# Kernel tuning notes

Measured on AMD Instinct MI355X. Metric: run time of the kernel, lower is better.

Reference implementation:

```python
import jax, jax.numpy as jnp
import numpy as np

DIM_HEAD = 128
HEADS = 16
SCALE = DIM_HEAD ** -0.5


def rotate_half(t):
    # '... (j d) -> ... j d' with j=2: split into first/second halves
    x1, x2 = jnp.split(t, 2, axis=-1)
    return jnp.concatenate((-x2, x1), axis=-1)


def apply_rope(pos, t):
    # pos: [n, d]; t: [..., n, d]
    return t * jnp.cos(pos) + rotate_half(t) * jnp.sin(pos)


def setup_inputs() -> dict:
    key = jax.random.key(0)
    k0, k1, k2, k3 = jax.random.split(key, 4)
    b, n, dim = 2, 2048, 2048
    inner = HEADS * DIM_HEAD
    return {
        "x": jax.random.normal(k0, (b, n, dim), jnp.float32),
        "Wq": jax.random.normal(k1, (dim, inner), jnp.float32) * 0.02,
        "Wkv": jax.random.normal(k2, (dim, 2 * DIM_HEAD), jnp.float32) * 0.02,
        "Wout": jax.random.normal(k3, (inner, dim), jnp.float32) * 0.02,
    }


def reference(x, Wq, Wkv, Wout):
    b, n, dim = x.shape
    # projections from the UN-normalized x (norm in original is dead code)
    q = x @ Wq                               # [b, n, h*d]
    kv = x @ Wkv                             # [b, n, 2d]
    k, v = jnp.split(kv, 2, axis=-1)         # each [b, n, d] (multi-query)
    q = q.reshape(b, n, HEADS, DIM_HEAD).transpose(0, 2, 1, 3)  # [b,h,n,d]

    # rotary positions
    inv_freq = 1.0 / (10000.0 ** (jnp.arange(0, DIM_HEAD, 2, dtype=jnp.float32) / DIM_HEAD))
    freqs = jnp.arange(n, dtype=jnp.float32)[:, None] * inv_freq[None, :]
    pos = jnp.concatenate((freqs, freqs), axis=-1)  # [n, d]

    q = apply_rope(pos, q) * SCALE
    k = apply_rope(pos, k)

    sim = jnp.einsum('bhid,bjd->bhij', q, k)  # [b,h,n,n]
    causal_mask = jnp.triu(jnp.ones((n, n), dtype=bool), 1)
    neg = -jnp.finfo(sim.dtype).max
    sim = jnp.where(causal_mask, neg, sim)
    sim = sim - jax.lax.stop_gradient(jnp.max(sim, axis=-1, keepdims=True))
    attn = jax.nn.softmax(sim, axis=-1)

    out = jnp.einsum('bhij,bjd->bhid', attn, v)          # [b,h,n,d]
    out = out.transpose(0, 2, 1, 3).reshape(b, n, HEADS * DIM_HEAD)
    return out @ Wout
```

## Files before the change

kernel.cpp:

```cpp
#include <hip/hip_runtime.h>
#include <hip/hip_bf16.h>
#include <cstddef>
#include <cstdint>

#define BATCH 2
#define SEQ   2048
#define DIM   2048
#define HEADS 16
#define DHEAD 128
#define INNER (HEADS * DHEAD)
#define MROWS (BATCH * SEQ)
#define ATT_SCALE 0.08838834764831845f
#define QK_SCALE (0.08838834764831845f * 1.4426950408889634f)
#define NEG_LOG2_10000_DIV64 (-13.287712379549449f / 64.0f)
#define M_HAT 12.0f

typedef __attribute__((ext_vector_type(8))) short short8;
typedef __attribute__((ext_vector_type(4))) short short4v;
typedef __attribute__((ext_vector_type(4))) float f32x4;

static __device__ __forceinline__ short f2bf(float x) {
    uint32_t u = __float_as_uint(x);
    uint32_t r = (u + 0x7fffu + ((u >> 16) & 1u)) >> 16;
    return (short)r;
}
static __device__ __forceinline__ float bf2f(short s) {
    return __uint_as_float(((uint32_t)(uint16_t)s) << 16);
}
static __device__ __forceinline__ short2 f2bf2(float a, float b) {
    __hip_bfloat162 h = __float22bfloat162_rn(make_float2(a, b));
    return *reinterpret_cast<short2*>(&h);
}

static __device__ __forceinline__ void glds16(const short* g, short* l) {
    __builtin_amdgcn_global_load_lds(
        (const __attribute__((address_space(1))) unsigned int*)g,
        (__attribute__((address_space(3))) unsigned int*)l, 16, 0, 0);
}

static __device__ __forceinline__ int swz_row(int r) {
    return (r & 3) | ((r >> 1) & 4);
}

static __device__ __forceinline__ void tcast_body(const float* __restrict__ W,
                                                  short* __restrict__ Wt,
                                                  int R, int C, int bx, int by,
                                                  int tid, float (*tile)[65]) {
    const int c0 = bx * 64, r0 = by * 64;
#pragma unroll
    for (int t = 0; t < 4; ++t) {
        int idx = tid + t * 256;
        int row = idx >> 4, col4 = idx & 15;
        float4 v = *(const float4*)&W[(size_t)(r0 + row) * C + c0 + col4 * 4];
        tile[row][col4 * 4 + 0] = v.x;
        tile[row][col4 * 4 + 1] = v.y;
        tile[row][col4 * 4 + 2] = v.z;
        tile[row][col4 * 4 + 3] = v.w;
    }
    __syncthreads();
#pragma unroll
    for (int t = 0; t < 4; ++t) {
        int idx = tid + t * 256;
        int r = idx >> 4, c4 = idx & 15;
        short2 s01 = f2bf2(tile[c4 * 4 + 0][r], tile[c4 * 4 + 1][r]);
        short2 s23 = f2bf2(tile[c4 * 4 + 2][r], tile[c4 * 4 + 3][r]);
        short4v s = {s01.x, s01.y, s23.x, s23.y};
        *(short4v*)&Wt[(size_t)(c0 + r) * R + r0 + c4 * 4] = s;
    }
}

__global__ __launch_bounds__(256) void prep(const float* __restrict__ x,
                                            short* __restrict__ xb,
                                            const float* __restrict__ Wq,
                                            short* __restrict__ Wt,
                                            const float* __restrict__ Wkv,
                                            short* __restrict__ Wkvt,
                                            const float* __restrict__ Wout,
                                            short* __restrict__ WtO,
                                            float2* __restrict__ lut) {
    __shared__ float tile[64][65];
    const int bid = blockIdx.x;
    const int tid = threadIdx.x;
    if (bid < 8192) {
        int i = bid * 256 + tid;
        float4 v = ((const float4*)x)[i];
        short2 s01 = f2bf2(v.x, v.y), s23 = f2bf2(v.z, v.w);
        short4v s = {s01.x, s01.y, s23.x, s23.y};
        ((short4v*)xb)[i] = s;
    } else if (bid < 9216) {
        int t = bid - 8192;
        tcast_body(Wq, Wt, DIM, INNER, t & 31, t >> 5, tid, tile);
    } else if (bid < 9344) {
        int t = bid - 9216;
        tcast_body(Wkv, Wkvt, DIM, 256, t & 3, t >> 2, tid, tile);
    } else if (bid < 10368) {
        int t = bid - 9344;
        tcast_body(Wout, WtO, INNER, DIM, t & 31, t >> 5, tid, tile);
    } else {
        int t = (bid - 10368) * 256 + tid;
        int pos = t >> 6, j = t & 63;
        float ang = (float)pos * exp2f((float)j * NEG_LOG2_10000_DIV64);
        lut[t] = make_float2(cosf(ang), sinf(ang));
    }
}

__global__ __launch_bounds__(256) void gemm_qkv(const short* __restrict__ A,
                                                const short* __restrict__ Bt,
                                                short* __restrict__ qout,
                                                short* __restrict__ kvout,
                                                short* __restrict__ kbout,
                                                const float2* __restrict__ lut) {
    __shared__ __align__(16) char smem[128 * 132 * 4];
    short* sA = (short*)smem;
    short* sB = (short*)(smem + 8192);
    float* tx = (float*)smem;
    const int K = DIM;

    const int tid = threadIdx.x;
    const int w = tid >> 6, lane = tid & 63;
    const int ln = lane & 15, qr = lane >> 4;
    const int flat = blockIdx.y * gridDim.x + blockIdx.x;
    const int wg = (flat & 7) * 72 + (flat >> 3);
    const int bm = (wg / 18) * 128, bn = (wg % 18) * 128;
    const int wm = (w >> 1) * 64, wn = (w & 1) * 64;

    const f32x4 zero4 = {0.f, 0.f, 0.f, 0.f};
    f32x4 acc[4][4];
#pragma unroll
    for (int mt = 0; mt < 4; ++mt)
#pragma unroll
        for (int nt = 0; nt < 4; ++nt) acc[mt][nt] = zero4;

    const int srow = lane >> 2;
    const short* pA = A + (size_t)(bm + w * 32 + srow) * K + (lane & 3) * 8;
    const short* pB = Bt + (size_t)(bn + w * 32 + srow) * K + (lane & 3) * 8;
    short* lA = &sA[(w * 32) * 32];
    short* lB = &sB[(w * 32) * 32];

    for (int k0 = 0; k0 < K; k0 += 32) {
        __syncthreads();
        glds16(pA + k0, lA);
        glds16(pA + k0 + (size_t)16 * K, lA + 512);
        glds16(pB + k0, lB);
        glds16(pB + k0 + (size_t)16 * K, lB + 512);
        __syncthreads();

        short8 af[4], bfr[4];
#pragma unroll
        for (int mt = 0; mt < 4; ++mt)
            af[mt] = *(const short8*)&sA[(wm + mt * 16 + ln) * 32 + qr * 8];
#pragma unroll
        for (int nt = 0; nt < 4; ++nt)
            bfr[nt] = *(const short8*)&sB[(wn + nt * 16 + ln) * 32 + qr * 8];
#pragma unroll
        for (int mt = 0; mt < 4; ++mt)
#pragma unroll
            for (int nt = 0; nt < 4; ++nt)
                acc[mt][nt] = __builtin_amdgcn_mfma_f32_16x16x32_bf16(
                    af[mt], bfr[nt], acc[mt][nt], 0, 0, 0);
    }

    if (bn <= INNER) {
        const float scale = (bn < INNER) ? QK_SCALE : 1.0f;
        __syncthreads();
#pragma unroll
        for (int mt = 0; mt < 4; ++mt)
#pragma unroll
            for (int nt = 0; nt < 4; ++nt)
#pragma unroll
                for (int r = 0; r < 4; ++r)
                    tx[(wm + mt * 16 + qr * 4 + r) * 132 + wn + nt * 16 + ln] =
                        acc[mt][nt][r];
        __syncthreads();
#pragma unroll
        for (int mt = 0; mt < 4; ++mt) {
#pragma unroll
            for (int nt = 0; nt < 4; ++nt) {
#pragma unroll
                for (int r = 0; r < 4; ++r) {
                    const int row_r = wm + mt * 16 + qr * 4 + r;
                    const int cn = wn + nt * 16 + ln;
                    const int pos = (bm + row_r) & (SEQ - 1);
                    const float own = acc[mt][nt][r];
                    const float partner = tx[row_r * 132 + (cn ^ 64)];
                    const float2 cs = lut[pos * 64 + (cn & 63)];
                    const float out = (wn == 0)
                                          ? (own * cs.x - partner * cs.y) * scale
                                          : (own * cs.x + partner * cs.y) * scale;
                    if (bn < INNER)
                        qout[(size_t)(bm + row_r) * INNER + bn + cn] = f2bf(out);
                    else
                        kbout[(size_t)(bm + row_r) * DHEAD + cn] = f2bf(out);
                }
            }
        }
    } else {
#pragma unroll
        for (int mt = 0; mt < 4; ++mt)
#pragma unroll
            for (int nt = 0; nt < 4; ++nt)
#pragma unroll
                for (int r = 0; r < 4; ++r)
                    kvout[(size_t)(bm + wm + mt * 16 + qr * 4 + r) * 256 + 128 +
                          wn + nt * 16 + ln] = f2bf(acc[mt][nt][r]);
    }
}

__global__ __launch_bounds__(256) void gemm_bt(const short* __restrict__ A,
                                               const short* __restrict__ Bt,
                                               float* __restrict__ C,
                                               int M, int N, int K) {
    __shared__ __align__(16) short sA[128 * 32];
    __shared__ __align__(16) short sB[128 * 32];

    const int tid = threadIdx.x;
    const int w = tid >> 6, lane = tid & 63;
    const int ln = lane & 15, qr = lane >> 4;
    const int flat = blockIdx.y * gridDim.x + blockIdx.x;
    const int wg = (flat & 7) * 64 + (flat >> 3);
    const int bm = (wg >> 4) * 128, bn = (wg & 15) * 128;
    const int wm = (w >> 1) * 64, wn = (w & 1) * 64;

    const f32x4 zero4 = {0.f, 0.f, 0.f, 0.f};
    f32x4 acc[4][4];
#pragma unroll
    for (int mt = 0; mt < 4; ++mt)
#pragma unroll
        for (int nt = 0; nt < 4; ++nt) acc[mt][nt] = zero4;

    const int srow = lane >> 2;
    const short* pA = A + (size_t)(bm + w * 32 + srow) * K + (lane & 3) * 8;
    const short* pB = Bt + (size_t)(bn + w * 32 + srow) * K + (lane & 3) * 8;
    short* lA = &sA[(w * 32) * 32];
    short* lB = &sB[(w * 32) * 32];

    for (int k0 = 0; k0 < K; k0 += 32) {
        __syncthreads();
        glds16(pA + k0, lA);
        glds16(pA + k0 + (size_t)16 * K, lA + 512);
        glds16(pB + k0, lB);
        glds16(pB + k0 + (size_t)16 * K, lB + 512);
        __syncthreads();

        short8 af[4], bfr[4];
#pragma unroll
        for (int mt = 0; mt < 4; ++mt)
            af[mt] = *(const short8*)&sA[(wm + mt * 16 + ln) * 32 + qr * 8];
#pragma unroll
        for (int nt = 0; nt < 4; ++nt)
            bfr[nt] = *(const short8*)&sB[(wn + nt * 16 + ln) * 32 + qr * 8];
#pragma unroll
        for (int mt = 0; mt < 4; ++mt)
#pragma unroll
            for (int nt = 0; nt < 4; ++nt)
                acc[mt][nt] = __builtin_amdgcn_mfma_f32_16x16x32_bf16(
                    af[mt], bfr[nt], acc[mt][nt], 0, 0, 0);
    }

#pragma unroll
    for (int mt = 0; mt < 4; ++mt)
#pragma unroll
        for (int nt = 0; nt < 4; ++nt)
#pragma unroll
            for (int r = 0; r < 4; ++r)
                C[(size_t)(bm + wm + mt * 16 + qr * 4 + r) * N +
                  bn + wn + nt * 16 + ln] = acc[mt][nt][r];
}

__global__ __launch_bounds__(256) void prep_kv(const short* __restrict__ kvbb,
                                               short* __restrict__ vt) {
    __shared__ float tile[64][65];
    const int bid = blockIdx.x;
    const int tid = threadIdx.x;
    const int b = bid >> 6;
    const int tile_id = bid & 63;
    const int p0 = (tile_id >> 1) * 64;
    const int d0 = (tile_id & 1) * 64;
#pragma unroll
    for (int t = 0; t < 16; ++t) {
        int idx = tid + t * 256;
        int row = idx >> 6, col = idx & 63;
        tile[row][col] = bf2f(kvbb[((size_t)(b * SEQ) + p0 + row) * 256 + 128 + d0 + col]);
    }
    __syncthreads();
#pragma unroll
    for (int t = 0; t < 16; ++t) {
        int idx = tid + t * 256;
        int r = idx >> 6, c = idx & 63;
        vt[((size_t)(b * DHEAD) + d0 + r) * SEQ + p0 + c] = f2bf(tile[c][r]);
    }
}

__global__ __launch_bounds__(512) void attn_mfma(const short* __restrict__ qb,
                                                 const short* __restrict__ kb,
                                                 const short* __restrict__ vt,
                                                 short* __restrict__ o) {
    __shared__ __align__(16) short sK[2][2][64 * 128];
    __shared__ __align__(16) short sV[2][2][128 * 64];
    __shared__ float lred[4][2][64];

    const int bid = blockIdx.x;
    const int p = bid & 7;
    const int bh = bid >> 3;
    const int h = bh & (HEADS - 1);
    const int b = bh >> 4;

    const int tid = threadIdx.x;
    const int w = tid >> 6;
    const int g = w >> 2;
    const int wg = w & 3;
    const int lane = tid & 63;
    const int ln = lane & 15;
    const int qr = lane >> 4;

    const short* kbase = kb + (size_t)b * SEQ * DHEAD;
    const short* vbase = vt + (size_t)b * DHEAD * SEQ;

    int offK[4], offV[4], ldsK[4], ldsV[4];
#pragma unroll
    for (int t = 0; t < 4; ++t) {
        int rk = wg * 16 + t * 4 + (lane >> 4);
        int ck = (lane & 15) ^ swz_row(rk);
        offK[t] = rk * DHEAD + ck * 8;
        ldsK[t] = (wg * 16 + t * 4) * 128;
        int rv = wg * 32 + t * 8 + (lane >> 3);
        int cv = (lane & 7) ^ swz_row(rv);
        offV[t] = rv * SEQ + cv * 8;
        ldsV[t] = (wg * 32 + t * 8) * 64;
    }

    for (int ph = 0; ph < 2; ++ph) {
        const int it = ph ? p : (15 - p);
        const int i0 = it * 128;
        const int njt = 2 * it + 2;
        const int half = njt >> 1;
        const int igmax = i0 + wg * 32 + 31;

        short8 qf[2][4];
#pragma unroll
        for (int qs = 0; qs < 2; ++qs) {
            const size_t qrow =
                ((size_t)(b * SEQ + i0 + wg * 32 + qs * 16 + ln)) * INNER + h * DHEAD;
#pragma unroll
            for (int ks = 0; ks < 4; ++ks)
                qf[qs][ks] = *(const short8*)&qb[qrow + ks * 32 + qr * 8];
        }

        const f32x4 zero4 = {0.f, 0.f, 0.f, 0.f};
        const f32x4 mhat4 = {-M_HAT, -M_HAT, -M_HAT, -M_HAT};
        f32x4 oa[2][8];
#pragma unroll
        for (int qs = 0; qs < 2; ++qs)
#pragma unroll
            for (int dt = 0; dt < 8; ++dt) oa[qs][dt] = zero4;
        float lsum[2] = {0.f, 0.f};

        __syncthreads();
        {
            const size_t kof = (size_t)g * 64 * DHEAD;
            const size_t vof = (size_t)g * 64;
#pragma unroll
            for (int t = 0; t < 4; ++t)
                glds16(kbase + kof + offK[t], &sK[g][0][ldsK[t]]);
#pragma unroll
            for (int t = 0; t < 4; ++t)
                glds16(vbase + vof + offV[t], &sV[g][0][ldsV[t]]);
        }

        for (int k = 0; k < half; ++k) {
            const int cur = k & 1;
            const int jt = 2 * k + g;
            __syncthreads();
            if (k + 1 < half) {
                const size_t kof = (size_t)(jt + 2) * 64 * DHEAD;
                const size_t vof = (size_t)(jt + 2) * 64;
#pragma unroll
                for (int t = 0; t < 4; ++t)
                    glds16(kbase + kof + offK[t], &sK[g][cur ^ 1][ldsK[t]]);
#pragma unroll
                for (int t = 0; t < 4; ++t)
                    glds16(vbase + vof + offV[t], &sV[g][cur ^ 1][ldsV[t]]);
            }
            if (jt * 64 > igmax) continue;

            f32x4 sacc[2][4];
#pragma unroll
            for (int qs = 0; qs < 2; ++qs)
#pragma unroll
                for (int nt = 0; nt < 4; ++nt) sacc[qs][nt] = mhat4;
            __builtin_amdgcn_s_setprio(1);
#pragma unroll
            for (int nt = 0; nt < 4; ++nt) {
                const int row = ((nt >> 1) << 5) + ((ln >> 2) << 3) +
                                ((nt & 1) << 2) + (ln & 3);
                const int sw = ln & 7;
#pragma unroll
                for (int ks = 0; ks < 4; ++ks) {
                    short8 kf = *(const short8*)&sK[g][cur][row * 128 + ((4 * ks + qr) ^ sw) * 8];
                    sacc[0][nt] = __builtin_amdgcn_mfma_f32_16x16x32_bf16(
                        kf, qf[0][ks], sacc[0][nt], 0, 0, 0);
                    sacc[1][nt] = __builtin_amdgcn_mfma_f32_16x16x32_bf16(
                        kf, qf[1][ks], sacc[1][nt], 0, 0, 0);
                }
            }
            __builtin_amdgcn_s_setprio(0);

            short8 pb[2][2];
#pragma unroll
            for (int qs = 0; qs < 2; ++qs) {
                const int ig = i0 + wg * 32 + qs * 16 + ln;
                if (jt * 64 + 63 > ig) {
#pragma unroll
                    for (int nt = 0; nt < 4; ++nt)
#pragma unroll
                        for (int r = 0; r < 4; ++r) {
                            int jg = jt * 64 + ((nt >> 1) << 5) + qr * 8 +
                                     ((nt & 1) << 2) + r;
                            if (jg > ig) sacc[qs][nt][r] = -3.0e38f;
                        }
                }
                float rs = 0.f;
                float pv[4][4];
#pragma unroll
                for (int nt = 0; nt < 4; ++nt)
#pragma unroll
                    for (int r = 0; r < 4; ++r) {
                        float e = exp2f(sacc[qs][nt][r]);
                        pv[nt][r] = e;
                        rs += e;
                    }
                rs += __shfl_xor(rs, 16);
                rs += __shfl_xor(rs, 32);
                lsum[qs] += rs;
#pragma unroll
                for (int kb2 = 0; kb2 < 2; ++kb2) {
                    short2* pp = (short2*)&pb[qs][kb2];
                    pp[0] = f2bf2(pv[2 * kb2][0], pv[2 * kb2][1]);
                    pp[1] = f2bf2(pv[2 * kb2][2], pv[2 * kb2][3]);
                    pp[2] = f2bf2(pv[2 * kb2 + 1][0], pv[2 * kb2 + 1][1]);
                    pp[3] = f2bf2(pv[2 * kb2 + 1][2], pv[2 * kb2 + 1][3]);
                }
            }

            __builtin_amdgcn_s_setprio(1);
#pragma unroll
            for (int kb2 = 0; kb2 < 2; ++kb2) {
#pragma unroll
                for (int dt = 0; dt < 8; ++dt) {
                    const int row = dt * 16 + ln;
                    short8 vf = *(const short8*)&sV[g][cur][row * 64 +
                        ((4 * kb2 + qr) ^ swz_row(row)) * 8];
                    oa[0][dt] = __builtin_amdgcn_mfma_f32_16x16x32_bf16(
                        vf, pb[0][kb2], oa[0][dt], 0, 0, 0);
                    oa[1][dt] = __builtin_amdgcn_mfma_f32_16x16x32_bf16(
                        vf, pb[1][kb2], oa[1][dt], 0, 0, 0);
                }
            }
            __builtin_amdgcn_s_setprio(0);
        }

        f32x4* cb = (f32x4*)&sK[1][0][0];
        __syncthreads();
        if (g == 1) {
#pragma unroll
            for (int dt = 0; dt < 8; ++dt)
                cb[dt * 256 + wg * 64 + lane] = oa[0][dt];
            lred[wg][0][lane] = lsum[0];
            lred[wg][1][lane] = lsum[1];
        }
        __syncthreads();
        if (g == 0) {
#pragma unroll
            for (int dt = 0; dt < 8; ++dt)
                oa[0][dt] += cb[dt * 256 + wg * 64 + lane];
            lsum[0] += lred[wg][0][lane];
            lsum[1] += lred[wg][1][lane];
        }
        __syncthreads();
        if (g == 1) {
#pragma unroll
            for (int dt = 0; dt < 8; ++dt)
                cb[dt * 256 + wg * 64 + lane] = oa[1][dt];
        }
        __syncthreads();
        if (g == 0) {
#pragma unroll
            for (int dt = 0; dt < 8; ++dt)
                oa[1][dt] += cb[dt * 256 + wg * 64 + lane];
#pragma unroll
            for (int qs = 0; qs < 2; ++qs) {
                const float invl = 1.f / lsum[qs];
                short* orow = o + ((size_t)(b * SEQ + i0 + wg * 32 + qs * 16 + ln)) * INNER +
                              h * DHEAD;
#pragma unroll
                for (int dt = 0; dt < 8; ++dt) {
                    short2 s01 = f2bf2(oa[qs][dt][0] * invl, oa[qs][dt][1] * invl);
                    short2 s23 = f2bf2(oa[qs][dt][2] * invl, oa[qs][dt][3] * invl);
                    short4v sv = {s01.x, s01.y, s23.x, s23.y};
                    *(short4v*)&orow[dt * 16 + qr * 4] = sv;
                }
            }
        }
    }
}

extern "C" void kernel_launch(void* const* d_in, const int* in_sizes, int n_in,
                              void* d_out, int out_size, void* d_ws, size_t ws_size,
                              hipStream_t stream) {
    const float* x    = (const float*)d_in[0];
    const float* Wq   = (const float*)d_in[1];
    const float* Wkv  = (const float*)d_in[2];
    const float* Wout = (const float*)d_in[3];
    float* out = (float*)d_out;

    short* xb    = (short*)d_ws;
    short* Wt    = xb + (size_t)MROWS * DIM;
    short* Wkvt  = Wt + (size_t)DIM * INNER;
    short* WtO   = Wkvt + (size_t)256 * DIM;
    short* qb    = WtO + (size_t)DIM * INNER;
    short* kvbb  = qb + (size_t)MROWS * INNER;
    short* kb    = kvbb + (size_t)MROWS * 256;
    short* vt    = kb + (size_t)MROWS * DHEAD;
    float2* lut  = (float2*)(vt + (size_t)BATCH * DHEAD * SEQ);
    short* ob    = xb;

    prep<<<10880, 256, 0, stream>>>(x, xb, Wq, Wt, Wkv, Wkvt, Wout, WtO, lut);
    gemm_qkv<<<dim3(18, 32), 256, 0, stream>>>(xb, Wt, qb, kvbb, kb, lut);
    prep_kv<<<128, 256, 0, stream>>>(kvbb, vt);
    attn_mfma<<<256, 512, 0, stream>>>(qb, kb, vt, ob);
    gemm_bt<<<dim3(16, 32), 256, 0, stream>>>(ob, WtO, out, MROWS, DIM, INNER);
}
```

Before: 323.4 us.

## Fuse V transpose into QKV GEMM epilogue and pair RoPE halves in registers

```diff
diff --git a/kernel.cpp b/kernel.cpp
--- a/kernel.cpp
+++ b/kernel.cpp
@@ -107,13 +107,11 @@
 __global__ __launch_bounds__(256) void gemm_qkv(const short* __restrict__ A,
                                                 const short* __restrict__ Bt,
                                                 short* __restrict__ qout,
-                                                short* __restrict__ kvout,
                                                 short* __restrict__ kbout,
+                                                short* __restrict__ vtout,
                                                 const float2* __restrict__ lut) {
-    __shared__ __align__(16) char smem[128 * 132 * 4];
-    short* sA = (short*)smem;
-    short* sB = (short*)(smem + 8192);
-    float* tx = (float*)smem;
+    __shared__ __align__(16) short sA[128 * 32];
+    __shared__ __align__(16) short sB[128 * 32];
     const int K = DIM;
 
     const int tid = threadIdx.x;
@@ -122,7 +120,8 @@
     const int flat = blockIdx.y * gridDim.x + blockIdx.x;
     const int wg = (flat & 7) * 72 + (flat >> 3);
     const int bm = (wg / 18) * 128, bn = (wg % 18) * 128;
-    const int wm = (w >> 1) * 64, wn = (w & 1) * 64;
+    const int wm = (w >> 1) * 64;
+    const int wn2 = (w & 1) * 32;
 
     const f32x4 zero4 = {0.f, 0.f, 0.f, 0.f};
     f32x4 acc[4][4];
@@ -150,8 +149,10 @@
         for (int mt = 0; mt < 4; ++mt)
             af[mt] = *(const short8*)&sA[(wm + mt * 16 + ln) * 32 + qr * 8];
 #pragma unroll
-        for (int nt = 0; nt < 4; ++nt)
-            bfr[nt] = *(const short8*)&sB[(wn + nt * 16 + ln) * 32 + qr * 8];
+        for (int nt = 0; nt < 4; ++nt) {
+            const int colr = wn2 + ((nt & 1) << 4) + ((nt >> 1) << 6) + ln;
+            bfr[nt] = *(const short8*)&sB[colr * 32 + qr * 8];
+        }
 #pragma unroll
         for (int mt = 0; mt < 4; ++mt)
 #pragma unroll
@@ -162,47 +163,47 @@
 
     if (bn <= INNER) {
         const float scale = (bn < INNER) ? QK_SCALE : 1.0f;
-        __syncthreads();
-#pragma unroll
-        for (int mt = 0; mt < 4; ++mt)
-#pragma unroll
-            for (int nt = 0; nt < 4; ++nt)
-#pragma unroll
-                for (int r = 0; r < 4; ++r)
-                    tx[(wm + mt * 16 + qr * 4 + r) * 132 + wn + nt * 16 + ln] =
-                        acc[mt][nt][r];
-        __syncthreads();
 #pragma unroll
         for (int mt = 0; mt < 4; ++mt) {
 #pragma unroll
+            for (int nt = 0; nt < 2; ++nt) {
+                const int d0 = wn2 + nt * 16 + ln;
+#pragma unroll
+                for (int r = 0; r < 4; ++r) {
+                    const int row = wm + mt * 16 + qr * 4 + r;
+                    const int pos = (bm + row) & (SEQ - 1);
+                    const float2 cs = lut[pos * 64 + d0];
+                    const float a = acc[mt][nt][r];
+                    const float b = acc[mt][nt + 2][r];
+                    const float lo = (a * cs.x - b * cs.y) * scale;
+                    const float hi = (b * cs.x + a * cs.y) * scale;
+                    if (bn < INNER) {
+                        short* q0 = qout + (size_t)(bm + row) * INNER + bn + d0;
+                        q0[0] = f2bf(lo);
+                        q0[64] = f2bf(hi);
+                    } else {
+                        short* k0p = kbout + (size_t)(bm + row) * DHEAD + d0;
+                        k0p[0] = f2bf(lo);
+                        k0p[64] = f2bf(hi);
+                    }
+                }
+            }
+        }
+    } else {
+        const int gb = bm >> 11;
+        const int pos_base = bm & (SEQ - 1);
+#pragma unroll
+        for (int mt = 0; mt < 4; ++mt) {
+#pragma unroll
             for (int nt = 0; nt < 4; ++nt) {
-#pragma unroll
-                for (int r = 0; r < 4; ++r) {
-                    const int row_r = wm + mt * 16 + qr * 4 + r;
-                    const int cn = wn + nt * 16 + ln;
-                    const int pos = (bm + row_r) & (SEQ - 1);
-                    const float own = acc[mt][nt][r];
-                    const float partner = tx[row_r * 132 + (cn ^ 64)];
-                    const float2 cs = lut[pos * 64 + (cn & 63)];
-                    const float out = (wn == 0)
-                                          ? (own * cs.x - partner * cs.y) * scale
-                                          : (own * cs.x + partner * cs.y) * scale;
-                    if (bn < INNER)
-                        qout[(size_t)(bm + row_r) * INNER + bn + cn] = f2bf(out);
-                    else
-                        kbout[(size_t)(bm + row_r) * DHEAD + cn] = f2bf(out);
-                }
-            }
-        }
-    } else {
-#pragma unroll
-        for (int mt = 0; mt < 4; ++mt)
-#pragma unroll
-            for (int nt = 0; nt < 4; ++nt)
-#pragma unroll
-                for (int r = 0; r < 4; ++r)
-                    kvout[(size_t)(bm + wm + mt * 16 + qr * 4 + r) * 256 + 128 +
-                          wn + nt * 16 + ln] = f2bf(acc[mt][nt][r]);
+                const int cn = wn2 + ((nt & 1) << 4) + ((nt >> 1) << 6) + ln;
+                const int pos0 = pos_base + wm + mt * 16 + qr * 4;
+                short2 s01 = f2bf2(acc[mt][nt][0], acc[mt][nt][1]);
+                short2 s23 = f2bf2(acc[mt][nt][2], acc[mt][nt][3]);
+                short4v sv = {s01.x, s01.y, s23.x, s23.y};
+                *(short4v*)&vtout[((size_t)gb * DHEAD + cn) * SEQ + pos0] = sv;
+            }
+        }
     }
 }
 
@@ -265,30 +266,6 @@
             for (int r = 0; r < 4; ++r)
                 C[(size_t)(bm + wm + mt * 16 + qr * 4 + r) * N +
                   bn + wn + nt * 16 + ln] = acc[mt][nt][r];
-}
-
-__global__ __launch_bounds__(256) void prep_kv(const short* __restrict__ kvbb,
-                                               short* __restrict__ vt) {
-    __shared__ float tile[64][65];
-    const int bid = blockIdx.x;
-    const int tid = threadIdx.x;
-    const int b = bid >> 6;
-    const int tile_id = bid & 63;
-    const int p0 = (tile_id >> 1) * 64;
-    const int d0 = (tile_id & 1) * 64;
-#pragma unroll
-    for (int t = 0; t < 16; ++t) {
-        int idx = tid + t * 256;
-        int row = idx >> 6, col = idx & 63;
-        tile[row][col] = bf2f(kvbb[((size_t)(b * SEQ) + p0 + row) * 256 + 128 + d0 + col]);
-    }
-    __syncthreads();
-#pragma unroll
-    for (int t = 0; t < 16; ++t) {
-        int idx = tid + t * 256;
-        int r = idx >> 6, c = idx & 63;
-        vt[((size_t)(b * DHEAD) + d0 + r) * SEQ + p0 + c] = f2bf(tile[c][r]);
-    }
 }
 
 __global__ __launch_bounds__(512) void attn_mfma(const short* __restrict__ qb,
@@ -518,15 +495,13 @@
     short* Wkvt  = Wt + (size_t)DIM * INNER;
     short* WtO   = Wkvt + (size_t)256 * DIM;
     short* qb    = WtO + (size_t)DIM * INNER;
-    short* kvbb  = qb + (size_t)MROWS * INNER;
-    short* kb    = kvbb + (size_t)MROWS * 256;
+    short* kb    = qb + (size_t)MROWS * INNER;
     short* vt    = kb + (size_t)MROWS * DHEAD;
     float2* lut  = (float2*)(vt + (size_t)BATCH * DHEAD * SEQ);
     short* ob    = xb;
 
     prep<<<10880, 256, 0, stream>>>(x, xb, Wq, Wt, Wkv, Wkvt, Wout, WtO, lut);
-    gemm_qkv<<<dim3(18, 32), 256, 0, stream>>>(xb, Wt, qb, kvbb, kb, lut);
-    prep_kv<<<128, 256, 0, stream>>>(kvbb, vt);
+    gemm_qkv<<<dim3(18, 32), 256, 0, stream>>>(xb, Wt, qb, kb, vt, lut);
     attn_mfma<<<256, 512, 0, stream>>>(qb, kb, vt, ob);
     gemm_bt<<<dim3(16, 32), 256, 0, stream>>>(ob, WtO, out, MROWS, DIM, INNER);
 }
```

Result: faster. 306.7 us (-5.1%).
